# Kernel tuning notes

Hardware: AMD Instinct MI355X
Metric: run time of the kernel (lower is better)

## Reference

```python
import jax, jax.numpy as jnp
import numpy as np

B, D, L, H = 8, 512, 2048, 8
DH = D // H
NEG = -1e30


def setup_inputs() -> dict:
    key = jax.random.key(0)
    k1, k2, k3, k4 = jax.random.split(key, 4)
    queries = jax.random.normal(k1, (B, D, L), dtype=jnp.float32)
    mask = jax.random.randint(k2, (B, L), 0, 2, dtype=jnp.int32)
    w_mem = jax.random.normal(k3, (2 * D, D), dtype=jnp.float32) * (1.0 / np.sqrt(D))
    w_q = jax.random.normal(k4, (D, D), dtype=jnp.float32) * (1.0 / np.sqrt(D))
    return {"queries": queries, "mask": mask, "w_mem": w_mem, "w_q": w_q}


def reference(queries, mask, w_mem, w_q):
    # 1x1 conv == pointwise GEMM over channel dim. queries: [B, D, L]
    memory = jnp.einsum('od,bdl->blo', w_mem, queries)  # [B, L, 2D]
    query = jnp.einsum('od,bdl->blo', w_q, queries)     # [B, L, D]

    def split_heads(x):  # [B, L, C] -> [B, H, L, C/H]
        b, l, c = x.shape
        return x.reshape(b, l, H, c // H).transpose(0, 2, 1, 3)

    k, v = memory[..., :D], memory[..., D:]
    Q = split_heads(query) * (DH ** -0.5)  # [B, H, L, DH]
    K = split_heads(k)
    V = split_heads(v)

    logits = jnp.einsum('bhqd,bhkd->bhqk', Q, K)  # [B, H, L, L]
    m = mask.astype(jnp.float32)[:, None, None, :]  # [B, 1, 1, L]
    logits = logits * m + (1.0 - m) * NEG
    weights = jax.nn.softmax(logits, axis=-1)
    x = jnp.einsum('bhqk,bhkd->bhqd', weights, V)  # [B, H, L, DH]
    # combine heads -> [B, L, D] -> transpose back to [B, D, L]
    out = x.transpose(0, 2, 1, 3).reshape(B, L, D).transpose(0, 2, 1)
    return out
```

## Files before the change

kernel.cpp:

```cpp
#include <hip/hip_runtime.h>
#include <hip/hip_bf16.h>

#define NB 8
#define ND 512
#define NL 2048
#define NH 8
#define NDH 64

typedef __attribute__((ext_vector_type(8))) short bf16x8;
typedef __attribute__((ext_vector_type(4))) float f32x4;

__device__ inline unsigned short f2bf(float x) {
    return (unsigned short)((__float_as_uint(x) + 0x8000u) >> 16);
}

__device__ inline float exp2_fast(float x) {
#if __has_builtin(__builtin_amdgcn_exp2f)
    return __builtin_amdgcn_exp2f(x);
#else
    return exp2f(x);
#endif
}

__global__ __launch_bounds__(256) void convert_w(
    const float* __restrict__ w_mem, const float* __restrict__ w_q,
    unsigned short* __restrict__ Wc)
{
    int idx = (blockIdx.x * 256 + threadIdx.x) * 8;
    int o = idx >> 9, k = idx & 511;
    const float* src;
    float sc;
    if (o < 1024) { src = w_mem + (size_t)o * ND + k; sc = 1.0f; }
    else          { src = w_q + (size_t)(o - 1024) * ND + k;
                    sc = 0.125f * 1.4426950408889634f; }
    float4 f0 = *(const float4*)src;
    float4 f1 = *(const float4*)(src + 4);
    ushort4 p0 = { f2bf(f0.x * sc), f2bf(f0.y * sc), f2bf(f0.z * sc), f2bf(f0.w * sc) };
    ushort4 p1 = { f2bf(f1.x * sc), f2bf(f1.y * sc), f2bf(f1.z * sc), f2bf(f1.w * sc) };
    *(ushort4*)(Wc + idx) = p0;
    *(ushort4*)(Wc + idx + 4) = p1;
}

__global__ __launch_bounds__(256) void convert_xt(
    const float* __restrict__ qin, unsigned short* __restrict__ Xt)
{
    __shared__ __align__(16) unsigned short T[64][72];
    const int b = blockIdx.z, d0 = blockIdx.y * 64, l0 = blockIdx.x * 64;
    const int t = threadIdx.x;
    const float* X = qin + ((size_t)b * ND + d0) * NL + l0;
    #pragma unroll
    for (int i = 0; i < 4; ++i) {
        int e = t + i * 256;
        int d = e >> 4, l4 = (e & 15) * 4;
        float4 v = *(const float4*)(X + (size_t)d * NL + l4);
        T[l4 + 0][d] = f2bf(v.x);
        T[l4 + 1][d] = f2bf(v.y);
        T[l4 + 2][d] = f2bf(v.z);
        T[l4 + 3][d] = f2bf(v.w);
    }
    __syncthreads();
    #pragma unroll
    for (int i = 0; i < 2; ++i) {
        int e = t + i * 256;
        int row = e >> 3, c8 = (e & 7) * 8;
        *(bf16x8*)(Xt + ((size_t)b * NL + l0 + row) * ND + d0 + c8) =
            *(const bf16x8*)&T[row][c8];
    }
}

__global__ __launch_bounds__(256, 3) void proj_mfma(
    const unsigned short* __restrict__ Wc,
    const unsigned short* __restrict__ Xt,
    unsigned short* __restrict__ Kh,
    unsigned short* __restrict__ Qh,
    unsigned short* __restrict__ Vt)
{
    __shared__ __align__(16) unsigned short As[128][72];
    __shared__ __align__(16) unsigned short Bs[128][72];

    const int b  = blockIdx.z;
    const int m0 = blockIdx.y * 128;
    const int n0 = blockIdx.x * 128;
    const int t  = threadIdx.x;
    const int w = t >> 6, lane = t & 63, quad = lane >> 4, lq = lane & 15;
    const int wo = (w >> 1) * 64, wl = (w & 1) * 64;

    f32x4 acc[4][4];
    #pragma unroll
    for (int im = 0; im < 4; ++im)
        #pragma unroll
        for (int in = 0; in < 4; ++in)
            acc[im][in] = (f32x4){0.f, 0.f, 0.f, 0.f};

    for (int k0 = 0; k0 < ND; k0 += 64) {
        __syncthreads();
        #pragma unroll
        for (int i = 0; i < 4; ++i) {
            int e = t + i * 256;
            int row = e >> 3, c8 = (e & 7) * 8;
            *(bf16x8*)&As[row][c8] =
                *(const bf16x8*)&Wc[(size_t)(m0 + row) * ND + k0 + c8];
            *(bf16x8*)&Bs[row][c8] =
                *(const bf16x8*)&Xt[((size_t)b * NL + n0 + row) * ND + k0 + c8];
        }
        __syncthreads();

        #pragma unroll
        for (int ks = 0; ks < 2; ++ks) {
            bf16x8 af[4], bf[4];
            #pragma unroll
            for (int im = 0; im < 4; ++im)
                af[im] = *(const bf16x8*)&As[wo + im * 16 + lq][ks * 32 + quad * 8];
            #pragma unroll
            for (int in = 0; in < 4; ++in)
                bf[in] = *(const bf16x8*)&Bs[wl + in * 16 + lq][ks * 32 + quad * 8];
            #pragma unroll
            for (int im = 0; im < 4; ++im)
                #pragma unroll
                for (int in = 0; in < 4; ++in)
                    acc[im][in] = __builtin_amdgcn_mfma_f32_16x16x32_bf16(
                        af[im], bf[in], acc[im][in], 0, 0, 0);
        }
    }

    const int reg = (m0 + wo) >> 9;
    if (reg != 1) {
        unsigned short* dst = (reg == 0) ? Kh : Qh;
        #pragma unroll
        for (int im = 0; im < 4; ++im) {
            int o  = (m0 + wo + im * 16 + quad * 4) & 511;
            int hh = o >> 6, dh = o & 63;
            #pragma unroll
            for (int in = 0; in < 4; ++in) {
                int l = n0 + wl + in * 16 + lq;
                ushort4 pk = { f2bf(acc[im][in][0]), f2bf(acc[im][in][1]),
                               f2bf(acc[im][in][2]), f2bf(acc[im][in][3]) };
                *(ushort4*)&dst[(((size_t)b * NH + hh) * NL + l) * NDH + dh] = pk;
            }
        }
    } else {
        #pragma unroll
        for (int im = 0; im < 4; ++im) {
            int o  = (m0 + wo + im * 16 + quad * 4) & 511;
            int hh = o >> 6, dh = o & 63;
            #pragma unroll
            for (int in = 0; in < 4; ++in) {
                int l  = n0 + wl + in * 16 + lq;
                int kk = l & 63;
                int s  = (kk & 32) | ((kk & 12) << 1) | ((kk & 16) >> 2) | (kk & 3);
                int lp = (l & ~63) | s;
                #pragma unroll
                for (int r = 0; r < 4; ++r)
                    Vt[(((size_t)b * NH + hh) * NDH + dh + r) * NL + lp] =
                        f2bf(acc[im][in][r]);
            }
        }
    }
}

__global__ __launch_bounds__(256, 2) void attn_mfma(
    const unsigned short* __restrict__ Qh,
    const unsigned short* __restrict__ Kh,
    const unsigned short* __restrict__ Vt,
    const int* __restrict__ maskp,
    float* __restrict__ out)
{
    __shared__ __align__(16) unsigned short Ks[64][72];
    __shared__ __align__(16) unsigned short Vts[64][72];
    __shared__ float mkf[64];

    const int q0 = blockIdx.x * 256;
    const int h = blockIdx.y, b = blockIdx.z;
    const int t = threadIdx.x;
    const int w = t >> 6, lane = t & 63, quad = lane >> 4, lq = lane & 15;

    const unsigned short* Qg = Qh + ((size_t)(b * NH + h)) * NL * NDH;
    const unsigned short* Kg = Kh + ((size_t)(b * NH + h)) * NL * NDH;
    const unsigned short* Vg = Vt + ((size_t)(b * NH + h)) * NDH * NL;

    bf16x8 qf[4][2];
    #pragma unroll
    for (int ni = 0; ni < 4; ++ni)
        #pragma unroll
        for (int ks = 0; ks < 2; ++ks)
            qf[ni][ks] = *(const bf16x8*)
                &Qg[(size_t)(q0 + w * 64 + ni * 16 + lq) * NDH + ks * 32 + quad * 8];

    f32x4 oacc[4][4];
    #pragma unroll
    for (int dm = 0; dm < 4; ++dm)
        #pragma unroll
        for (int ni = 0; ni < 4; ++ni)
            oacc[dm][ni] = (f32x4){0.f, 0.f, 0.f, 0.f};
    float lsum[4] = {0.f, 0.f, 0.f, 0.f};

    const int srow = t >> 3;
    const int scol = (t & 7) * 8;

    bf16x8 pk[2], pv[2];
    int mreg = 0;
    #pragma unroll
    for (int i = 0; i < 2; ++i) {
        pk[i] = *(const bf16x8*)&Kg[(size_t)(srow + 32 * i) * NDH + scol];
        pv[i] = *(const bf16x8*)&Vg[(size_t)(srow + 32 * i) * NL + scol];
    }
    if (t < 64) mreg = maskp[b * NL + t];

    for (int k0 = 0; k0 < NL; k0 += 64) {
        __syncthreads();
        #pragma unroll
        for (int i = 0; i < 2; ++i) {
            *(bf16x8*)&Ks[srow + 32 * i][scol]  = pk[i];
            *(bf16x8*)&Vts[srow + 32 * i][scol] = pv[i];
        }
        if (t < 64) mkf[t] = mreg ? 0.0f : -1e30f;
        __syncthreads();

        int kn = (k0 + 64 < NL) ? k0 + 64 : k0;
        #pragma unroll
        for (int i = 0; i < 2; ++i) {
            pk[i] = *(const bf16x8*)&Kg[(size_t)(kn + srow + 32 * i) * NDH + scol];
            pv[i] = *(const bf16x8*)&Vg[(size_t)(srow + 32 * i) * NL + kn + scol];
        }
        if (t < 64) mreg = maskp[b * NL + kn + t];

        f32x4 sacc[4][4];
        #pragma unroll
        for (int mi = 0; mi < 4; ++mi)
            #pragma unroll
            for (int ni = 0; ni < 4; ++ni)
                sacc[mi][ni] = (f32x4){0.f, 0.f, 0.f, 0.f};
        #pragma unroll
        for (int ks = 0; ks < 2; ++ks) {
            bf16x8 kf[4];
            #pragma unroll
            for (int mi = 0; mi < 4; ++mi)
                kf[mi] = *(const bf16x8*)&Ks[mi * 16 + lq][ks * 32 + quad * 8];
            #pragma unroll
            for (int mi = 0; mi < 4; ++mi)
                #pragma unroll
                for (int ni = 0; ni < 4; ++ni)
                    sacc[mi][ni] = __builtin_amdgcn_mfma_f32_16x16x32_bf16(
                        kf[mi], qf[ni][ks], sacc[mi][ni], 0, 0, 0);
        }

        bf16x8 pf[4][2];
        #pragma unroll
        for (int mi = 0; mi < 4; ++mi) {
            float4 mk4 = *(const float4*)&mkf[mi * 16 + quad * 4];
            float mk[4] = {mk4.x, mk4.y, mk4.z, mk4.w};
            const int ks = mi >> 1, j0 = (mi & 1) * 4;
            #pragma unroll
            for (int ni = 0; ni < 4; ++ni)
                #pragma unroll
                for (int r = 0; r < 4; ++r) {
                    float e = exp2_fast(sacc[mi][ni][r] + mk[r]);
                    lsum[ni] += e;
                    pf[ni][ks][j0 + r] = (short)f2bf(e);
                }
        }

        #pragma unroll
        for (int ks = 0; ks < 2; ++ks) {
            bf16x8 vf[4];
            #pragma unroll
            for (int dm = 0; dm < 4; ++dm)
                vf[dm] = *(const bf16x8*)&Vts[dm * 16 + lq][ks * 32 + quad * 8];
            #pragma unroll
            for (int dm = 0; dm < 4; ++dm)
                #pragma unroll
                for (int ni = 0; ni < 4; ++ni)
                    oacc[dm][ni] = __builtin_amdgcn_mfma_f32_16x16x32_bf16(
                        vf[dm], pf[ni][ks], oacc[dm][ni], 0, 0, 0);
        }
    }

    #pragma unroll
    for (int ni = 0; ni < 4; ++ni) {
        lsum[ni] += __shfl_xor(lsum[ni], 16);
        lsum[ni] += __shfl_xor(lsum[ni], 32);
        lsum[ni] = 1.0f / lsum[ni];
    }
    #pragma unroll
    for (int dm = 0; dm < 4; ++dm)
        #pragma unroll
        for (int ni = 0; ni < 4; ++ni)
            #pragma unroll
            for (int r = 0; r < 4; ++r) {
                int dh = dm * 16 + quad * 4 + r;
                int l  = q0 + w * 64 + ni * 16 + lq;
                out[((size_t)b * ND + h * NDH + dh) * NL + l] =
                    oacc[dm][ni][r] * lsum[ni];
            }
}

extern "C" void kernel_launch(void* const* d_in, const int* in_sizes, int n_in,
                              void* d_out, int out_size, void* d_ws, size_t ws_size,
                              hipStream_t stream) {
    const float* queries = (const float*)d_in[0];
    const int*   maskp   = (const int*)d_in[1];
    const float* w_mem   = (const float*)d_in[2];
    const float* w_q     = (const float*)d_in[3];
    float* out = (float*)d_out;

    const size_t headElems = (size_t)NB * NH * NL * NDH;
    unsigned short* Kh = (unsigned short*)d_ws;
    unsigned short* Vt = Kh + headElems;
    unsigned short* Qh = Vt + headElems;
    unsigned short* Wc = Qh + headElems;
    unsigned short* Xt = Wc + (size_t)1536 * ND;

    convert_w<<<384, 256, 0, stream>>>(w_mem, w_q, Wc);

    dim3 gx(NL / 64, ND / 64, NB);
    convert_xt<<<gx, 256, 0, stream>>>(queries, Xt);

    dim3 g1(NL / 128, 1536 / 128, NB);
    proj_mfma<<<g1, 256, 0, stream>>>(Wc, Xt, Kh, Qh, Vt);

    dim3 g2(NL / 256, NH, NB);
    attn_mfma<<<g2, 256, 0, stream>>>(Qh, Kh, Vt, maskp, out);
}
```

Before: 204.0 us.

## Fold mask into V, async LDS loads with swizzle, double-buffer attention tiles

Several changes land together. The key mask is applied by zeroing masked V columns in the projection epilogue, and an extra all-ones-under-mask row is appended to V so the softmax denominator comes out of the PV MFMA. That removes the per-element mask add and the lsum accumulation and shuffles. Both GEMM kernels now use global_load_lds direct-to-LDS copies with an XOR-swizzled, unpadded layout, and attention double-buffers its K/V tiles while the grid is remapped to a 1D order with head innermost. Bf16 packing now uses a perm instruction. The trade-offs are an extra MFMA row block (a fifth of the PV work), an extra kernel launch to write the mask row, and skipping the max subtraction in softmax, which relies on the logits staying small.

```diff
diff --git a/kernel.cpp b/kernel.cpp
--- a/kernel.cpp
+++ b/kernel.cpp
@@ -6,20 +6,34 @@
 #define NL 2048
 #define NH 8
 #define NDH 64
+#define VROWS 72
 
 typedef __attribute__((ext_vector_type(8))) short bf16x8;
 typedef __attribute__((ext_vector_type(4))) float f32x4;
-
-__device__ inline unsigned short f2bf(float x) {
+typedef __attribute__((ext_vector_type(4))) unsigned int u32x4;
+
+__device__ __forceinline__ unsigned short f2bf(float x) {
     return (unsigned short)((__float_as_uint(x) + 0x8000u) >> 16);
 }
 
-__device__ inline float exp2_fast(float x) {
+__device__ __forceinline__ float exp2_fast(float x) {
 #if __has_builtin(__builtin_amdgcn_exp2f)
     return __builtin_amdgcn_exp2f(x);
 #else
     return exp2f(x);
 #endif
+}
+
+__device__ __forceinline__ unsigned int pack_bf16(float a, float b) {
+    unsigned int ua = __float_as_uint(a) + 0x8000u;
+    unsigned int ub = __float_as_uint(b) + 0x8000u;
+    return __builtin_amdgcn_perm(ub, ua, 0x07060302u);
+}
+
+__device__ __forceinline__ void async16(void* lds, const void* g) {
+    __builtin_amdgcn_global_load_lds(
+        (const __attribute__((address_space(1))) unsigned int*)g,
+        (__attribute__((address_space(3))) unsigned int*)lds, 16, 0, 0);
 }
 
 __global__ __launch_bounds__(256) void convert_w(
@@ -68,15 +82,32 @@
     }
 }
 
+__global__ __launch_bounds__(256) void write_vmask(
+    const int* __restrict__ maskp, unsigned short* __restrict__ Vt)
+{
+    const int bh = blockIdx.x;
+    const int b = bh >> 3;
+    unsigned short* base = Vt + (size_t)bh * VROWS * NL;
+    unsigned short* row64 = base + (size_t)64 * NL;
+    for (int kk = threadIdx.x; kk < NL; kk += 256) {
+        int s  = (kk & 32) | ((kk & 12) << 1) | ((kk & 16) >> 2) | (kk & 3);
+        int lp = (kk & ~63) | s;
+        row64[lp] = maskp[b * NL + kk] ? (unsigned short)0x3F80 : (unsigned short)0;
+    }
+    unsigned short* z = base + (size_t)65 * NL;
+    for (int i = threadIdx.x; i < 7 * NL; i += 256) z[i] = 0;
+}
+
 __global__ __launch_bounds__(256, 3) void proj_mfma(
     const unsigned short* __restrict__ Wc,
     const unsigned short* __restrict__ Xt,
+    const int* __restrict__ maskp,
     unsigned short* __restrict__ Kh,
     unsigned short* __restrict__ Qh,
     unsigned short* __restrict__ Vt)
 {
-    __shared__ __align__(16) unsigned short As[128][72];
-    __shared__ __align__(16) unsigned short Bs[128][72];
+    __shared__ __align__(16) unsigned short As[128 * 64];
+    __shared__ __align__(16) unsigned short Bs[128 * 64];
 
     const int b  = blockIdx.z;
     const int m0 = blockIdx.y * 128;
@@ -84,6 +115,8 @@
     const int t  = threadIdx.x;
     const int w = t >> 6, lane = t & 63, quad = lane >> 4, lq = lane & 15;
     const int wo = (w >> 1) * 64, wl = (w & 1) * 64;
+    const int lr = lane >> 3;
+    const int cbsw = (lane & 7) ^ lr;
 
     f32x4 acc[4][4];
     #pragma unroll
@@ -94,32 +127,39 @@
 
     for (int k0 = 0; k0 < ND; k0 += 64) {
         __syncthreads();
-        #pragma unroll
-        for (int i = 0; i < 4; ++i) {
-            int e = t + i * 256;
-            int row = e >> 3, c8 = (e & 7) * 8;
-            *(bf16x8*)&As[row][c8] =
-                *(const bf16x8*)&Wc[(size_t)(m0 + row) * ND + k0 + c8];
-            *(bf16x8*)&Bs[row][c8] =
-                *(const bf16x8*)&Xt[((size_t)b * NL + n0 + row) * ND + k0 + c8];
+        #pragma unroll 2
+        for (int i = w; i < 32; i += 4) {
+            if (i < 16) {
+                int R = i * 8;
+                async16(&As[R * 64],
+                        Wc + (size_t)(m0 + R + lr) * ND + k0 + cbsw * 8);
+            } else {
+                int R = (i - 16) * 8;
+                async16(&Bs[R * 64],
+                        Xt + ((size_t)b * NL + n0 + R + lr) * ND + k0 + cbsw * 8);
+            }
         }
         __syncthreads();
 
         #pragma unroll
         for (int ks = 0; ks < 2; ++ks) {
-            bf16x8 af[4], bf[4];
-            #pragma unroll
-            for (int im = 0; im < 4; ++im)
-                af[im] = *(const bf16x8*)&As[wo + im * 16 + lq][ks * 32 + quad * 8];
-            #pragma unroll
-            for (int in = 0; in < 4; ++in)
-                bf[in] = *(const bf16x8*)&Bs[wl + in * 16 + lq][ks * 32 + quad * 8];
+            bf16x8 af[4], bfr[4];
+            #pragma unroll
+            for (int im = 0; im < 4; ++im) {
+                int r = wo + im * 16 + lq;
+                af[im] = *(const bf16x8*)&As[r * 64 + (((ks * 4 + quad) ^ (lq & 7)) * 8)];
+            }
+            #pragma unroll
+            for (int in = 0; in < 4; ++in) {
+                int r = wl + in * 16 + lq;
+                bfr[in] = *(const bf16x8*)&Bs[r * 64 + (((ks * 4 + quad) ^ (lq & 7)) * 8)];
+            }
             #pragma unroll
             for (int im = 0; im < 4; ++im)
                 #pragma unroll
                 for (int in = 0; in < 4; ++in)
                     acc[im][in] = __builtin_amdgcn_mfma_f32_16x16x32_bf16(
-                        af[im], bf[in], acc[im][in], 0, 0, 0);
+                        af[im], bfr[in], acc[im][in], 0, 0, 0);
         }
     }
 
@@ -139,6 +179,10 @@
             }
         }
     } else {
+        float mv[4];
+        #pragma unroll
+        for (int in = 0; in < 4; ++in)
+            mv[in] = (float)maskp[b * NL + (n0 + wl + in * 16 + lq)];
         #pragma unroll
         for (int im = 0; im < 4; ++im) {
             int o  = (m0 + wo + im * 16 + quad * 4) & 511;
@@ -151,8 +195,8 @@
                 int lp = (l & ~63) | s;
                 #pragma unroll
                 for (int r = 0; r < 4; ++r)
-                    Vt[(((size_t)b * NH + hh) * NDH + dh + r) * NL + lp] =
-                        f2bf(acc[im][in][r]);
+                    Vt[(((size_t)(b * NH + hh)) * VROWS + dh + r) * NL + lp] =
+                        f2bf(acc[im][in][r] * mv[in]);
             }
         }
     }
@@ -162,21 +206,34 @@
     const unsigned short* __restrict__ Qh,
     const unsigned short* __restrict__ Kh,
     const unsigned short* __restrict__ Vt,
-    const int* __restrict__ maskp,
     float* __restrict__ out)
 {
-    __shared__ __align__(16) unsigned short Ks[64][72];
-    __shared__ __align__(16) unsigned short Vts[64][72];
-    __shared__ float mkf[64];
-
-    const int q0 = blockIdx.x * 256;
-    const int h = blockIdx.y, b = blockIdx.z;
+    __shared__ __align__(16) unsigned short Ks2[2][64 * 64];
+    __shared__ __align__(16) unsigned short Vs2[2][80 * 64];
+
+    const int id = blockIdx.x;
+    const int h  = id & 7;
+    const int b  = (id >> 3) & 7;
+    const int q0 = (id >> 6) * 256;
     const int t = threadIdx.x;
     const int w = t >> 6, lane = t & 63, quad = lane >> 4, lq = lane & 15;
+    const int lr = lane >> 3;
+    const int cbsw = (lane & 7) ^ lr;
 
     const unsigned short* Qg = Qh + ((size_t)(b * NH + h)) * NL * NDH;
     const unsigned short* Kg = Kh + ((size_t)(b * NH + h)) * NL * NDH;
-    const unsigned short* Vg = Vt + ((size_t)(b * NH + h)) * NDH * NL;
+    const unsigned short* Vg = Vt + ((size_t)(b * NH + h)) * VROWS * NL;
+
+    #pragma unroll 2
+    for (int i = w; i < 17; i += 4) {
+        if (i < 8) {
+            int R = i * 8;
+            async16(&Ks2[0][R * 64], Kg + (size_t)(R + lr) * NDH + cbsw * 8);
+        } else {
+            int R = (i - 8) * 8;
+            async16(&Vs2[0][R * 64], Vg + (size_t)(R + lr) * NL + cbsw * 8);
+        }
+    }
 
     bf16x8 qf[4][2];
     #pragma unroll
@@ -186,43 +243,35 @@
             qf[ni][ks] = *(const bf16x8*)
                 &Qg[(size_t)(q0 + w * 64 + ni * 16 + lq) * NDH + ks * 32 + quad * 8];
 
-    f32x4 oacc[4][4];
-    #pragma unroll
-    for (int dm = 0; dm < 4; ++dm)
+    f32x4 oacc[5][4];
+    #pragma unroll
+    for (int dm = 0; dm < 5; ++dm)
         #pragma unroll
         for (int ni = 0; ni < 4; ++ni)
             oacc[dm][ni] = (f32x4){0.f, 0.f, 0.f, 0.f};
-    float lsum[4] = {0.f, 0.f, 0.f, 0.f};
-
-    const int srow = t >> 3;
-    const int scol = (t & 7) * 8;
-
-    bf16x8 pk[2], pv[2];
-    int mreg = 0;
-    #pragma unroll
-    for (int i = 0; i < 2; ++i) {
-        pk[i] = *(const bf16x8*)&Kg[(size_t)(srow + 32 * i) * NDH + scol];
-        pv[i] = *(const bf16x8*)&Vg[(size_t)(srow + 32 * i) * NL + scol];
-    }
-    if (t < 64) mreg = maskp[b * NL + t];
-
+
+    int cur = 0;
     for (int k0 = 0; k0 < NL; k0 += 64) {
         __syncthreads();
-        #pragma unroll
-        for (int i = 0; i < 2; ++i) {
-            *(bf16x8*)&Ks[srow + 32 * i][scol]  = pk[i];
-            *(bf16x8*)&Vts[srow + 32 * i][scol] = pv[i];
-        }
-        if (t < 64) mkf[t] = mreg ? 0.0f : -1e30f;
-        __syncthreads();
-
-        int kn = (k0 + 64 < NL) ? k0 + 64 : k0;
-        #pragma unroll
-        for (int i = 0; i < 2; ++i) {
-            pk[i] = *(const bf16x8*)&Kg[(size_t)(kn + srow + 32 * i) * NDH + scol];
-            pv[i] = *(const bf16x8*)&Vg[(size_t)(srow + 32 * i) * NL + kn + scol];
-        }
-        if (t < 64) mreg = maskp[b * NL + kn + t];
+
+        if (k0 + 64 < NL) {
+            const int kn = k0 + 64, nb = cur ^ 1;
+            #pragma unroll 2
+            for (int i = w; i < 17; i += 4) {
+                if (i < 8) {
+                    int R = i * 8;
+                    async16(&Ks2[nb][R * 64],
+                            Kg + (size_t)(kn + R + lr) * NDH + cbsw * 8);
+                } else {
+                    int R = (i - 8) * 8;
+                    async16(&Vs2[nb][R * 64],
+                            Vg + (size_t)(R + lr) * NL + kn + cbsw * 8);
+                }
+            }
+        }
+
+        const unsigned short* KsB = Ks2[cur];
+        const unsigned short* VsB = Vs2[cur];
 
         f32x4 sacc[4][4];
         #pragma unroll
@@ -235,7 +284,8 @@
             bf16x8 kf[4];
             #pragma unroll
             for (int mi = 0; mi < 4; ++mi)
-                kf[mi] = *(const bf16x8*)&Ks[mi * 16 + lq][ks * 32 + quad * 8];
+                kf[mi] = *(const bf16x8*)
+                    &KsB[(mi * 16 + lq) * 64 + (((ks * 4 + quad) ^ (lq & 7)) * 8)];
             #pragma unroll
             for (int mi = 0; mi < 4; ++mi)
                 #pragma unroll
@@ -244,43 +294,44 @@
                         kf[mi], qf[ni][ks], sacc[mi][ni], 0, 0, 0);
         }
 
-        bf16x8 pf[4][2];
+        u32x4 pfu[4][2];
         #pragma unroll
         for (int mi = 0; mi < 4; ++mi) {
-            float4 mk4 = *(const float4*)&mkf[mi * 16 + quad * 4];
-            float mk[4] = {mk4.x, mk4.y, mk4.z, mk4.w};
-            const int ks = mi >> 1, j0 = (mi & 1) * 4;
-            #pragma unroll
-            for (int ni = 0; ni < 4; ++ni)
-                #pragma unroll
-                for (int r = 0; r < 4; ++r) {
-                    float e = exp2_fast(sacc[mi][ni][r] + mk[r]);
-                    lsum[ni] += e;
-                    pf[ni][ks][j0 + r] = (short)f2bf(e);
-                }
+            const int ks = mi >> 1, jp = (mi & 1) * 2;
+            #pragma unroll
+            for (int ni = 0; ni < 4; ++ni) {
+                float e0 = exp2_fast(sacc[mi][ni][0]);
+                float e1 = exp2_fast(sacc[mi][ni][1]);
+                float e2 = exp2_fast(sacc[mi][ni][2]);
+                float e3 = exp2_fast(sacc[mi][ni][3]);
+                pfu[ni][ks][jp + 0] = pack_bf16(e0, e1);
+                pfu[ni][ks][jp + 1] = pack_bf16(e2, e3);
+            }
         }
 
         #pragma unroll
         for (int ks = 0; ks < 2; ++ks) {
-            bf16x8 vf[4];
-            #pragma unroll
-            for (int dm = 0; dm < 4; ++dm)
-                vf[dm] = *(const bf16x8*)&Vts[dm * 16 + lq][ks * 32 + quad * 8];
-            #pragma unroll
-            for (int dm = 0; dm < 4; ++dm)
+            bf16x8 vf[5];
+            #pragma unroll
+            for (int dm = 0; dm < 5; ++dm)
+                vf[dm] = *(const bf16x8*)
+                    &VsB[(dm * 16 + lq) * 64 + (((ks * 4 + quad) ^ (lq & 7)) * 8)];
+            #pragma unroll
+            for (int dm = 0; dm < 5; ++dm)
                 #pragma unroll
                 for (int ni = 0; ni < 4; ++ni)
                     oacc[dm][ni] = __builtin_amdgcn_mfma_f32_16x16x32_bf16(
-                        vf[dm], pf[ni][ks], oacc[dm][ni], 0, 0, 0);
-        }
-    }
-
-    #pragma unroll
-    for (int ni = 0; ni < 4; ++ni) {
-        lsum[ni] += __shfl_xor(lsum[ni], 16);
-        lsum[ni] += __shfl_xor(lsum[ni], 32);
-        lsum[ni] = 1.0f / lsum[ni];
-    }
+                        vf[dm], __builtin_bit_cast(bf16x8, pfu[ni][ks]),
+                        oacc[dm][ni], 0, 0, 0);
+        }
+        cur ^= 1;
+    }
+
+    float inv[4];
+    #pragma unroll
+    for (int ni = 0; ni < 4; ++ni)
+        inv[ni] = 1.0f / __shfl(oacc[4][ni][0], lq);
+
     #pragma unroll
     for (int dm = 0; dm < 4; ++dm)
         #pragma unroll
@@ -290,7 +341,7 @@
                 int dh = dm * 16 + quad * 4 + r;
                 int l  = q0 + w * 64 + ni * 16 + lq;
                 out[((size_t)b * ND + h * NDH + dh) * NL + l] =
-                    oacc[dm][ni][r] * lsum[ni];
+                    oacc[dm][ni][r] * inv[ni];
             }
 }
 
@@ -303,10 +354,11 @@
     const float* w_q     = (const float*)d_in[3];
     float* out = (float*)d_out;
 
-    const size_t headElems = (size_t)NB * NH * NL * NDH;
+    const size_t headElems  = (size_t)NB * NH * NL * NDH;
+    const size_t vElems     = (size_t)NB * NH * VROWS * NL;
     unsigned short* Kh = (unsigned short*)d_ws;
     unsigned short* Vt = Kh + headElems;
-    unsigned short* Qh = Vt + headElems;
+    unsigned short* Qh = Vt + vElems;
     unsigned short* Wc = Qh + headElems;
     unsigned short* Xt = Wc + (size_t)1536 * ND;
 
@@ -315,9 +367,10 @@
     dim3 gx(NL / 64, ND / 64, NB);
     convert_xt<<<gx, 256, 0, stream>>>(queries, Xt);
 
+    write_vmask<<<NB * NH, 256, 0, stream>>>(maskp, Vt);
+
     dim3 g1(NL / 128, 1536 / 128, NB);
-    proj_mfma<<<g1, 256, 0, stream>>>(Wc, Xt, Kh, Qh, Vt);
-
-    dim3 g2(NL / 256, NH, NB);
-    attn_mfma<<<g2, 256, 0, stream>>>(Qh, Kh, Vt, maskp, out);
-}
+    proj_mfma<<<g1, 256, 0, stream>>>(Wc, Xt, maskp, Kh, Qh, Vt);
+
+    attn_mfma<<<512, 256, 0, stream>>>(Qh, Kh, Vt, out);
+}
```

Result: no change. 204.6 us (+0.3%).
